# Kernel tuning notes

Hardware: AMD Instinct MI355X
Metric: run time of the kernel (lower is better)

The kernel has to match this reference:

```python
import jax, jax.numpy as jnp
import numpy as np

B, D, K = 32, 64, 26      # batch, n_objects, per-object feature dim
QST = 256                  # question embedding size
G = [512, 512, 512, 512, 512, 512, 28]  # g_layers (last = n_answers)
IN = 2 * K                 # in_size = concat(x_i, x_j)
AGG = 4                    # aggregation + question injection position


def setup_inputs() -> dict:
    key = jax.random.key(0)
    ks = jax.random.split(key, 2 + 2 * len(G))
    inp = {
        "x": jax.random.normal(ks[0], (B, D, K), jnp.float32),
        "qst": jax.random.normal(ks[1], (B, QST), jnp.float32),
    }
    prev = IN
    for i, g in enumerate(G):
        d_in = prev + (QST if i == AGG else 0)
        inp[f"W{i}"] = jax.random.normal(ks[2 + 2 * i], (g, d_in), jnp.float32) * (1.0 / np.sqrt(d_in))
        inp[f"b{i}"] = jnp.zeros((g,), jnp.float32)
        prev = g
    return inp


def reference(x, qst, W0, b0, W1, b1, W2, b2, W3, b3, W4, b4, W5, b5, W6, b6):
    b, d, k = x.shape
    # all ordered pairs: x_full[b, p, q] = [x[b, q], x[b, p]]  (matches torch repeat/cat order)
    xi = jnp.broadcast_to(x[:, None, :, :], (b, d, d, k))
    xj = jnp.broadcast_to(x[:, :, None, :], (b, d, d, k))
    h = jnp.concatenate([xi, xj], axis=-1).reshape(b * d * d, 2 * k)
    Ws = [W0, W1, W2, W3, W4, W5, W6]
    bs = [b0, b1, b2, b3, b4, b5, b6]
    n = len(Ws)
    for i in range(n):
        if i == AGG:
            # sum-aggregation over all d^2 pairs, then question injection
            h = h.reshape(b, d * d, h.shape[-1]).sum(axis=1)  # [b, g]
            h = jnp.concatenate([h, qst], axis=1)             # [b, g+qst]
        h = h @ Ws[i].T + bs[i]
        if i != n - 1:
            h = jax.nn.relu(h)
    return jax.nn.log_softmax(h, axis=1)
```

## Files before the change

### kernel.cpp

```cpp
#include <hip/hip_runtime.h>
#include <math.h>


typedef __attribute__((ext_vector_type(8))) short bf16x8;
typedef __attribute__((ext_vector_type(4))) float f32x4;
typedef __attribute__((ext_vector_type(4))) unsigned int u32x4;

__device__ __forceinline__ unsigned short f2bf(float f) {
    union { float f; unsigned u; } x; x.f = f;
    unsigned r = x.u + 0x7fffu + ((x.u >> 16) & 1u);
    return (unsigned short)(r >> 16);
}

#define NP_WP   786432
#define NP_W0P  32768
#define NP_W4T  393216
#define NP_W5T  262144
#define NP_TOTAL (NP_WP + NP_W0P + NP_W4T + NP_W5T)
__global__ void k_prep(const float* __restrict__ W1, const float* __restrict__ W2,
                       const float* __restrict__ W3, const float* __restrict__ W0,
                       const float* __restrict__ W4, const float* __restrict__ W5,
                       unsigned short* __restrict__ Wp,
                       unsigned short* __restrict__ W0p,
                       float* __restrict__ W4v,
                       float* __restrict__ W5v)
{
    int f = blockIdx.x * 256 + threadIdx.x;
    if (f < NP_WP) {
        int l = f >> 18, r = f & 262143;
        int n = r >> 9, k = r & 511;
        const float* W = (l == 0) ? W1 : (l == 1) ? W2 : W3;
        float v = W[r];
        int wv = n >> 6, jj = (n >> 4) & 3, i16 = n & 15;
        int s = k >> 5, q4 = (k >> 3) & 3, j = k & 7;
        int lane = q4 * 16 + i16;
        Wp[(size_t)l * 262144 + ((((wv * 16 + s) * 4 + jj) * 64 + lane) << 3) + j] = f2bf(v);
    } else if (f < NP_WP + NP_W0P) {
        int g = f - NP_WP;
        int n = g >> 6, k = g & 63;
        float v = (k < 52) ? W0[n * 52 + k] : 0.f;
        int wv = n >> 6, jj = (n >> 4) & 3, i16 = n & 15;
        int s = k >> 5, q4 = (k >> 3) & 3, j = k & 7;
        int lane = q4 * 16 + i16;
        W0p[((((wv * 2 + s) * 4 + jj) * 64 + lane) << 3) + j] = f2bf(v);
    } else if (f < NP_WP + NP_W0P + NP_W4T) {
        int g = f - (NP_WP + NP_W0P);
        int o = g / 768, k = g % 768;
        W4v[(size_t)((k >> 2) * 512 + o) * 4 + (k & 3)] = W4[g];
    } else {
        int g = f - (NP_WP + NP_W0P + NP_W4T);
        int o = g >> 9, k = g & 511;
        W5v[(size_t)((k >> 2) * 512 + o) * 4 + (k & 3)] = W5[g];
    }
}

__device__ __forceinline__ void store_h(const f32x4 (&acc)[4][4], const float* __restrict__ bl,
                                        unsigned short* hsm, int wave, int i16, int q4, int lane)
{
    char* base = (char*)hsm;
    #pragma unroll
    for (int j = 0; j < 4; ++j) {
        int col = (wave * 4 + j) * 16 + i16;
        int g = col >> 3;
        int e = g & 7;
        float bb = bl[col];
        #pragma unroll
        for (int mt = 0; mt < 4; ++mt) {
            #pragma unroll
            for (int r = 0; r < 4; ++r) {
                int row = mt * 16 + q4 * 4 + r;
                float v = fmaxf(acc[mt][j][r] + bb, 0.f);
                unsigned hv = f2bf(v);
                unsigned sw = (unsigned)__builtin_amdgcn_update_dpp(0, (int)hv, 0xB1, 0xF, 0xF, true);
                if ((lane & 1) == 0) {
                    int slot = row ^ e;
                    *(unsigned*)(base + g * 1024 + slot * 16 + ((col & 7) << 1)) = hv | (sw << 16);
                }
            }
        }
    }
}

#define CLUSTER(AV0, AV1, AV2, AV3, BV, JJ)                                              \
    __builtin_amdgcn_s_setprio(1);                                                      \
    acc[0][JJ] = __builtin_amdgcn_mfma_f32_16x16x32_bf16(AV0, BV, acc[0][JJ], 0, 0, 0); \
    acc[1][JJ] = __builtin_amdgcn_mfma_f32_16x16x32_bf16(AV1, BV, acc[1][JJ], 0, 0, 0); \
    acc[2][JJ] = __builtin_amdgcn_mfma_f32_16x16x32_bf16(AV2, BV, acc[2][JJ], 0, 0, 0); \
    acc[3][JJ] = __builtin_amdgcn_mfma_f32_16x16x32_bf16(AV3, BV, acc[3][JJ], 0, 0, 0); \
    __builtin_amdgcn_s_setprio(0);                                                      \
    __builtin_amdgcn_sched_barrier(0);

__global__ __launch_bounds__(512, 2) void k_fused(
    const float* __restrict__ x,
    const unsigned short* __restrict__ Wp,
    const unsigned short* __restrict__ W0p,
    const float* __restrict__ b0, const float* __restrict__ b1,
    const float* __restrict__ b2, const float* __restrict__ b3,
    float* __restrict__ P)
{
    __shared__ __align__(16) unsigned short hsm[64 * 512];
    __shared__ __align__(16) unsigned short xs[8 * 64 * 8];
    int t = threadIdx.x;
    int blk = blockIdx.x;
    int b = blk >> 6, p = blk & 63;

    {
        int row = t >> 3, gr = t & 7;
        const float* xq = x + (size_t)(b * 64 + row) * 26;
        const float* xp = x + (size_t)(b * 64 + p) * 26;
        unsigned w[4];
        #pragma unroll
        for (int h = 0; h < 4; ++h) {
            int k0 = gr * 8 + h * 2;
            int k1 = k0 + 1;
            float f0 = (k0 < 26) ? xq[k0] : (k0 < 52 ? xp[k0 - 26] : 0.f);
            float f1 = (k1 < 26) ? xq[k1] : (k1 < 52 ? xp[k1 - 26] : 0.f);
            w[h] = (unsigned)f2bf(f0) | ((unsigned)f2bf(f1) << 16);
        }
        *(u32x4*)((char*)xs + gr * 1024 + ((row ^ gr) << 4)) = (u32x4){w[0], w[1], w[2], w[3]};
    }

    int wave = t >> 6, lane = t & 63;
    int i16 = lane & 15, q4 = lane >> 4;

    f32x4 acc[4][4];

    __syncthreads();

    {
        #pragma unroll
        for (int mt = 0; mt < 4; ++mt)
            #pragma unroll
            for (int j = 0; j < 4; ++j)
                acc[mt][j] = (f32x4){0.f, 0.f, 0.f, 0.f};
        const unsigned short* Bb0 = W0p + wave * 4096 + lane * 8;
        const char* xb = (const char*)xs;
        #pragma unroll
        for (int s = 0; s < 2; ++s) {
            bf16x8 bfr[4];
            #pragma unroll
            for (int j = 0; j < 4; ++j)
                bfr[j] = *(const bf16x8*)(Bb0 + s * 2048 + j * 512);
            int g = s * 4 + q4;
            const char* A0 = xb + g * 1024 + ((i16 ^ g) << 4);
            #pragma unroll
            for (int mt = 0; mt < 4; ++mt) {
                bf16x8 a = *(const bf16x8*)(A0 + mt * 256);
                #pragma unroll
                for (int j = 0; j < 4; ++j)
                    acc[mt][j] = __builtin_amdgcn_mfma_f32_16x16x32_bf16(a, bfr[j], acc[mt][j], 0, 0, 0);
            }
        }
        store_h(acc, b0, hsm, wave, i16, q4, lane);
    }

    int A_even = (q4 << 10) + ((i16 ^ q4) << 4);
    const char* hbe = (const char*)hsm + A_even;
    const char* hbo = (const char*)hsm + 4096 + (A_even ^ 64);

    #pragma unroll 1
    for (int l = 0; l < 3; ++l) {
        const float* bl = (l == 0) ? b1 : (l == 1) ? b2 : b3;
        const unsigned short* Bb = Wp + (size_t)l * 262144 + wave * 32768 + lane * 8;

        bf16x8 X0 = *(const bf16x8*)(Bb);
        bf16x8 X1 = *(const bf16x8*)(Bb + 512);
        bf16x8 X2 = *(const bf16x8*)(Bb + 1024);
        bf16x8 X3 = *(const bf16x8*)(Bb + 1536);
        bf16x8 Y0 = *(const bf16x8*)(Bb + 2048);
        bf16x8 Y1 = *(const bf16x8*)(Bb + 2560);
        bf16x8 Y2 = *(const bf16x8*)(Bb + 3072);
        bf16x8 Y3 = *(const bf16x8*)(Bb + 3584);

        __syncthreads();

        #pragma unroll
        for (int mt = 0; mt < 4; ++mt)
            #pragma unroll
            for (int j = 0; j < 4; ++j)
                acc[mt][j] = (f32x4){0.f, 0.f, 0.f, 0.f};

        bf16x8 aE0 = *(const bf16x8*)(hbe);
        bf16x8 aE1 = *(const bf16x8*)(hbe + 256);
        bf16x8 aE2 = *(const bf16x8*)(hbe + 512);
        bf16x8 aE3 = *(const bf16x8*)(hbe + 768);
        bf16x8 aO0, aO1, aO2, aO3;

        #pragma unroll 1
        for (int s = 0; s < 16; s += 2) {
            {
                const unsigned short* BX = Bb + ((s + 2 < 16) ? (s + 2) : 14) * 2048;
                const char* po = hbo + (s << 12);
                CLUSTER(aE0, aE1, aE2, aE3, X0, 0)
                X0 = *(const bf16x8*)(BX);
                aO0 = *(const bf16x8*)(po);
                aO1 = *(const bf16x8*)(po + 256);
                CLUSTER(aE0, aE1, aE2, aE3, X1, 1)
                X1 = *(const bf16x8*)(BX + 512);
                aO2 = *(const bf16x8*)(po + 512);
                aO3 = *(const bf16x8*)(po + 768);
                CLUSTER(aE0, aE1, aE2, aE3, X2, 2)
                X2 = *(const bf16x8*)(BX + 1024);
                CLUSTER(aE0, aE1, aE2, aE3, X3, 3)
                X3 = *(const bf16x8*)(BX + 1536);
            }
            {
                const unsigned short* BY = Bb + ((s + 3 < 16) ? (s + 3) : 15) * 2048;
                const char* pe = hbe + ((s + 2 < 16 ? s + 2 : 14) << 12);
                CLUSTER(aO0, aO1, aO2, aO3, Y0, 0)
                Y0 = *(const bf16x8*)(BY);
                aE0 = *(const bf16x8*)(pe);
                aE1 = *(const bf16x8*)(pe + 256);
                CLUSTER(aO0, aO1, aO2, aO3, Y1, 1)
                Y1 = *(const bf16x8*)(BY + 512);
                aE2 = *(const bf16x8*)(pe + 512);
                aE3 = *(const bf16x8*)(pe + 768);
                CLUSTER(aO0, aO1, aO2, aO3, Y2, 2)
                Y2 = *(const bf16x8*)(BY + 1024);
                CLUSTER(aO0, aO1, aO2, aO3, Y3, 3)
                Y3 = *(const bf16x8*)(BY + 1536);
            }
        }
        __syncthreads();

        if (l < 2) {
            store_h(acc, bl, hsm, wave, i16, q4, lane);
        } else {
            #pragma unroll
            for (int j = 0; j < 4; ++j) {
                int col = (wave * 4 + j) * 16 + i16;
                float bb = bl[col];
                float sum = 0.f;
                #pragma unroll
                for (int mt = 0; mt < 4; ++mt)
                    #pragma unroll
                    for (int r = 0; r < 4; ++r)
                        sum += fmaxf(acc[mt][j][r] + bb, 0.f);
                sum += __shfl_xor(sum, 16);
                sum += __shfl_xor(sum, 32);
                if (q4 == 0) P[(size_t)blk * 512 + col] = sum;
            }
        }
    }
}

__global__ __launch_bounds__(1024) void k_tail(
    const float* __restrict__ P, const float* __restrict__ qst,
    const float* __restrict__ W4v, const float* __restrict__ b4,
    const float* __restrict__ W5v, const float* __restrict__ b5,
    const float* __restrict__ W6, const float* __restrict__ b6,
    float* __restrict__ out)
{
    int b = blockIdx.x, t = threadIdx.x;
    __shared__ __align__(16) float z[768];
    __shared__ __align__(16) float ps[1024];
    __shared__ __align__(16) float h4[512];
    __shared__ float h5[512];
    __shared__ float logits[28];
    __shared__ float red[2];

    if (t < 512) {
        float s = 0.f;
        const float* Pb = P + (size_t)b * 64 * 512 + t;
        #pragma unroll 8
        for (int c = 0; c < 64; ++c) s += Pb[c * 512];
        z[t] = s;
    } else if (t < 768) {
        z[t] = qst[b * 256 + (t - 512)];
    }
    __syncthreads();
    {
        int o = t & 511, hf = t >> 9;
        float acc = 0.f;
        const float4* Wv = (const float4*)W4v;
        const float4* z4 = (const float4*)z;
        #pragma unroll 4
        for (int kb = hf * 96; kb < hf * 96 + 96; ++kb) {
            float4 w = Wv[kb * 512 + o];
            float4 zz = z4[kb];
            acc = fmaf(w.x, zz.x, acc);
            acc = fmaf(w.y, zz.y, acc);
            acc = fmaf(w.z, zz.z, acc);
            acc = fmaf(w.w, zz.w, acc);
        }
        ps[t] = acc;
    }
    __syncthreads();
    if (t < 512) h4[t] = fmaxf(ps[t] + ps[t + 512] + b4[t], 0.f);
    __syncthreads();
    {
        int o = t & 511, hf = t >> 9;
        float acc = 0.f;
        const float4* Wv = (const float4*)W5v;
        const float4* h44 = (const float4*)h4;
        #pragma unroll 4
        for (int kb = hf * 64; kb < hf * 64 + 64; ++kb) {
            float4 w = Wv[kb * 512 + o];
            float4 hh = h44[kb];
            acc = fmaf(w.x, hh.x, acc);
            acc = fmaf(w.y, hh.y, acc);
            acc = fmaf(w.z, hh.z, acc);
            acc = fmaf(w.w, hh.w, acc);
        }
        ps[t] = acc;
    }
    __syncthreads();
    if (t < 512) h5[t] = fmaxf(ps[t] + ps[t + 512] + b5[t], 0.f);
    __syncthreads();
    {
        int o = t >> 5, c = t & 31;
        if (o < 28) {
            float acc = 0.f;
            for (int k = c; k < 512; k += 32) acc = fmaf(W6[o * 512 + k], h5[k], acc);
            acc += __shfl_xor(acc, 1);
            acc += __shfl_xor(acc, 2);
            acc += __shfl_xor(acc, 4);
            acc += __shfl_xor(acc, 8);
            acc += __shfl_xor(acc, 16);
            if (c == 0) logits[o] = acc + b6[o];
        }
    }
    __syncthreads();
    if (t == 0) {
        float mx = -1e30f;
        for (int cc = 0; cc < 28; ++cc) mx = fmaxf(mx, logits[cc]);
        float se = 0.f;
        for (int cc = 0; cc < 28; ++cc) se += expf(logits[cc] - mx);
        red[0] = mx; red[1] = logf(se);
    }
    __syncthreads();
    if (t < 28) out[b * 28 + t] = logits[t] - red[0] - red[1];
}

extern "C" void kernel_launch(void* const* d_in, const int* in_sizes, int n_in,
                              void* d_out, int out_size, void* d_ws, size_t ws_size,
                              hipStream_t stream)
{
    const float* x   = (const float*)d_in[0];
    const float* qst = (const float*)d_in[1];
    const float* W0  = (const float*)d_in[2];
    const float* b0  = (const float*)d_in[3];
    const float* W1  = (const float*)d_in[4];
    const float* b1  = (const float*)d_in[5];
    const float* W2  = (const float*)d_in[6];
    const float* b2  = (const float*)d_in[7];
    const float* W3  = (const float*)d_in[8];
    const float* b3  = (const float*)d_in[9];
    const float* W4  = (const float*)d_in[10];
    const float* b4  = (const float*)d_in[11];
    const float* W5  = (const float*)d_in[12];
    const float* b5  = (const float*)d_in[13];
    const float* W6  = (const float*)d_in[14];
    const float* b6  = (const float*)d_in[15];
    float* out = (float*)d_out;

    char* ws = (char*)d_ws;
    unsigned short* Wp  = (unsigned short*)(ws);
    unsigned short* W0p = (unsigned short*)(ws + 1572864);
    float*          W4v = (float*)(ws + 1638400);
    float*          W5v = (float*)(ws + 3211264);
    float*          P   = (float*)(ws + 4259840);

    k_prep <<<NP_TOTAL / 256, 256, 0, stream>>>(W1, W2, W3, W0, W4, W5,
                                                Wp, W0p, W4v, W5v);
    k_fused<<<2048, 512, 0, stream>>>(x, Wp, W0p, b0, b1, b2, b3, P);
    k_tail <<<32, 1024, 0, stream>>>(P, qst, W4v, b4, W5v, b5, W6, b6, out);
}
```

Measured before the change: 324.9 us.

## Deepen register prefetch pipeline to four stages and use packed bf16 convert

The inner GEMM loop for layers 1-3 now keeps four sets of weight and activation register fragments in flight instead of two. It prefetches weights four k-steps ahead and activations three steps ahead, so global and LDS load latency is better hidden behind MFMA clusters. store_h now uses the hardware v_cvt_pk_bf16_f32 instruction instead of manual rounding and bit packing. The deeper pipeline roughly doubles the VGPRs held for fragments, which could cause spills or limit occupancy at 2 blocks of 512 threads.

New measurement: 367.5 us. 13.1% more time.

```diff
diff --git a/kernel.cpp b/kernel.cpp
--- a/kernel.cpp
+++ b/kernel.cpp
@@ -64,17 +64,20 @@
         int g = col >> 3;
         int e = g & 7;
         float bb = bl[col];
+        char* colbase = base + g * 1024 + ((col & 7) << 1);
         #pragma unroll
         for (int mt = 0; mt < 4; ++mt) {
             #pragma unroll
             for (int r = 0; r < 4; ++r) {
                 int row = mt * 16 + q4 * 4 + r;
                 float v = fmaxf(acc[mt][j][r] + bb, 0.f);
-                unsigned hv = f2bf(v);
-                unsigned sw = (unsigned)__builtin_amdgcn_update_dpp(0, (int)hv, 0xB1, 0xF, 0xF, true);
+                int vi = __float_as_int(v);
+                int swi = __builtin_amdgcn_update_dpp(0, vi, 0xB1, 0xF, 0xF, true);
                 if ((lane & 1) == 0) {
+                    unsigned pk;
+                    asm("v_cvt_pk_bf16_f32 %0, %1, %2" : "=v"(pk) : "v"(vi), "v"(swi));
                     int slot = row ^ e;
-                    *(unsigned*)(base + g * 1024 + slot * 16 + ((col & 7) << 1)) = hv | (sw << 16);
+                    *(unsigned*)(colbase + slot * 16) = pk;
                 }
             }
         }
@@ -90,6 +93,20 @@
     __builtin_amdgcn_s_setprio(0);                                                      \
     __builtin_amdgcn_sched_barrier(0);
 
+#define BODY(cA0,cA1,cA2,cA3, cB0,cB1,cB2,cB3, nA0,nA1,nA2,nA3, An, Bn)  \
+    CLUSTER(cA0,cA1,cA2,cA3, cB0, 0)                                     \
+    cB0 = *(const bf16x8*)(Bn);                                          \
+    nA0 = *(const bf16x8*)(An);                                          \
+    nA1 = *(const bf16x8*)((An) + 256);                                  \
+    CLUSTER(cA0,cA1,cA2,cA3, cB1, 1)                                     \
+    cB1 = *(const bf16x8*)((Bn) + 512);                                  \
+    nA2 = *(const bf16x8*)((An) + 512);                                  \
+    nA3 = *(const bf16x8*)((An) + 768);                                  \
+    CLUSTER(cA0,cA1,cA2,cA3, cB2, 2)                                     \
+    cB2 = *(const bf16x8*)((Bn) + 1024);                                 \
+    CLUSTER(cA0,cA1,cA2,cA3, cB3, 3)                                     \
+    cB3 = *(const bf16x8*)((Bn) + 1536);
+
 __global__ __launch_bounds__(512, 2) void k_fused(
     const float* __restrict__ x,
     const unsigned short* __restrict__ Wp,
@@ -156,21 +173,29 @@
 
     int A_even = (q4 << 10) + ((i16 ^ q4) << 4);
     const char* hbe = (const char*)hsm + A_even;
-    const char* hbo = (const char*)hsm + 4096 + (A_even ^ 64);
+    const char* hbo = (const char*)hsm + (A_even ^ 64);
 
     #pragma unroll 1
     for (int l = 0; l < 3; ++l) {
         const float* bl = (l == 0) ? b1 : (l == 1) ? b2 : b3;
         const unsigned short* Bb = Wp + (size_t)l * 262144 + wave * 32768 + lane * 8;
 
-        bf16x8 X0 = *(const bf16x8*)(Bb);
-        bf16x8 X1 = *(const bf16x8*)(Bb + 512);
-        bf16x8 X2 = *(const bf16x8*)(Bb + 1024);
-        bf16x8 X3 = *(const bf16x8*)(Bb + 1536);
-        bf16x8 Y0 = *(const bf16x8*)(Bb + 2048);
-        bf16x8 Y1 = *(const bf16x8*)(Bb + 2560);
-        bf16x8 Y2 = *(const bf16x8*)(Bb + 3072);
-        bf16x8 Y3 = *(const bf16x8*)(Bb + 3584);
+        bf16x8 bX0 = *(const bf16x8*)(Bb);
+        bf16x8 bX1 = *(const bf16x8*)(Bb + 512);
+        bf16x8 bX2 = *(const bf16x8*)(Bb + 1024);
+        bf16x8 bX3 = *(const bf16x8*)(Bb + 1536);
+        bf16x8 bY0 = *(const bf16x8*)(Bb + 2048);
+        bf16x8 bY1 = *(const bf16x8*)(Bb + 2560);
+        bf16x8 bY2 = *(const bf16x8*)(Bb + 3072);
+        bf16x8 bY3 = *(const bf16x8*)(Bb + 3584);
+        bf16x8 bZ0 = *(const bf16x8*)(Bb + 4096);
+        bf16x8 bZ1 = *(const bf16x8*)(Bb + 4608);
+        bf16x8 bZ2 = *(const bf16x8*)(Bb + 5120);
+        bf16x8 bZ3 = *(const bf16x8*)(Bb + 5632);
+        bf16x8 bW0 = *(const bf16x8*)(Bb + 6144);
+        bf16x8 bW1 = *(const bf16x8*)(Bb + 6656);
+        bf16x8 bW2 = *(const bf16x8*)(Bb + 7168);
+        bf16x8 bW3 = *(const bf16x8*)(Bb + 7680);
 
         __syncthreads();
 
@@ -180,46 +205,42 @@
             for (int j = 0; j < 4; ++j)
                 acc[mt][j] = (f32x4){0.f, 0.f, 0.f, 0.f};
 
-        bf16x8 aE0 = *(const bf16x8*)(hbe);
-        bf16x8 aE1 = *(const bf16x8*)(hbe + 256);
-        bf16x8 aE2 = *(const bf16x8*)(hbe + 512);
-        bf16x8 aE3 = *(const bf16x8*)(hbe + 768);
-        bf16x8 aO0, aO1, aO2, aO3;
+        bf16x8 aA0 = *(const bf16x8*)(hbe);
+        bf16x8 aA1 = *(const bf16x8*)(hbe + 256);
+        bf16x8 aA2 = *(const bf16x8*)(hbe + 512);
+        bf16x8 aA3 = *(const bf16x8*)(hbe + 768);
+        const char* a1p = hbo + 4096;
+        bf16x8 aB0 = *(const bf16x8*)(a1p);
+        bf16x8 aB1 = *(const bf16x8*)(a1p + 256);
+        bf16x8 aB2 = *(const bf16x8*)(a1p + 512);
+        bf16x8 aB3 = *(const bf16x8*)(a1p + 768);
+        const char* a2p = hbe + 8192;
+        bf16x8 aC0 = *(const bf16x8*)(a2p);
+        bf16x8 aC1 = *(const bf16x8*)(a2p + 256);
+        bf16x8 aC2 = *(const bf16x8*)(a2p + 512);
+        bf16x8 aC3 = *(const bf16x8*)(a2p + 768);
+        bf16x8 aD0, aD1, aD2, aD3;
 
         #pragma unroll 1
-        for (int s = 0; s < 16; s += 2) {
-            {
-                const unsigned short* BX = Bb + ((s + 2 < 16) ? (s + 2) : 14) * 2048;
-                const char* po = hbo + (s << 12);
-                CLUSTER(aE0, aE1, aE2, aE3, X0, 0)
-                X0 = *(const bf16x8*)(BX);
-                aO0 = *(const bf16x8*)(po);
-                aO1 = *(const bf16x8*)(po + 256);
-                CLUSTER(aE0, aE1, aE2, aE3, X1, 1)
-                X1 = *(const bf16x8*)(BX + 512);
-                aO2 = *(const bf16x8*)(po + 512);
-                aO3 = *(const bf16x8*)(po + 768);
-                CLUSTER(aE0, aE1, aE2, aE3, X2, 2)
-                X2 = *(const bf16x8*)(BX + 1024);
-                CLUSTER(aE0, aE1, aE2, aE3, X3, 3)
-                X3 = *(const bf16x8*)(BX + 1536);
-            }
-            {
-                const unsigned short* BY = Bb + ((s + 3 < 16) ? (s + 3) : 15) * 2048;
-                const char* pe = hbe + ((s + 2 < 16 ? s + 2 : 14) << 12);
-                CLUSTER(aO0, aO1, aO2, aO3, Y0, 0)
-                Y0 = *(const bf16x8*)(BY);
-                aE0 = *(const bf16x8*)(pe);
-                aE1 = *(const bf16x8*)(pe + 256);
-                CLUSTER(aO0, aO1, aO2, aO3, Y1, 1)
-                Y1 = *(const bf16x8*)(BY + 512);
-                aE2 = *(const bf16x8*)(pe + 512);
-                aE3 = *(const bf16x8*)(pe + 768);
-                CLUSTER(aO0, aO1, aO2, aO3, Y2, 2)
-                Y2 = *(const bf16x8*)(BY + 1024);
-                CLUSTER(aO0, aO1, aO2, aO3, Y3, 3)
-                Y3 = *(const bf16x8*)(BY + 1536);
-            }
+        for (int s = 0; s < 16; s += 4) {
+            int sA1 = (s + 4 < 16) ? s + 4 : 12;
+            int sA2 = (s + 5 < 16) ? s + 5 : 13;
+            int sA3 = (s + 6 < 16) ? s + 6 : 14;
+            int sB0 = sA1, sB1 = sA2, sB2 = sA3;
+            int sB3 = (s + 7 < 16) ? s + 7 : 15;
+            const char* An0 = hbo + ((s + 3) << 12);
+            const char* An1 = hbe + (sA1 << 12);
+            const char* An2 = hbo + (sA2 << 12);
+            const char* An3 = hbe + (sA3 << 12);
+            const unsigned short* Bn0 = Bb + sB0 * 2048;
+            const unsigned short* Bn1 = Bb + sB1 * 2048;
+            const unsigned short* Bn2 = Bb + sB2 * 2048;
+            const unsigned short* Bn3 = Bb + sB3 * 2048;
+
+            BODY(aA0,aA1,aA2,aA3, bX0,bX1,bX2,bX3, aD0,aD1,aD2,aD3, An0, Bn0)
+            BODY(aB0,aB1,aB2,aB3, bY0,bY1,bY2,bY3, aA0,aA1,aA2,aA3, An1, Bn1)
+            BODY(aC0,aC1,aC2,aC3, bZ0,bZ1,bZ2,bZ3, aB0,aB1,aB2,aB3, An2, Bn2)
+            BODY(aD0,aD1,aD2,aD3, bW0,bW1,bW2,bW3, aC0,aC1,aC2,aC3, An3, Bn3)
         }
         __syncthreads();
 
```

## Double per-block row tile to 128 pairs to halve weight traffic per MFMA

Applied to the files above, without the earlier changes.

Each block now handles two p values (128 rows) instead of one, doubling the accumulator tile to 8x4 MFMA tiles per wave so every loaded weight fragment feeds twice as many MFMAs. The LDS activation buffer doubles to 128 KB, the inner loop is rescheduled to stream A fragments per row tile, and the grid is halved to 1024 blocks. The bf16 packing in store_h now uses a single v_cvt_pk_bf16_f32 instruction. This raises register and LDS pressure, which may cut occupancy below two blocks per CU.

After: 497.4 us. 1.53x slower.

```diff
diff --git a/kernel.cpp b/kernel.cpp
--- a/kernel.cpp
+++ b/kernel.cpp
@@ -54,7 +54,7 @@
     }
 }
 
-__device__ __forceinline__ void store_h(const f32x4 (&acc)[4][4], const float* __restrict__ bl,
+__device__ __forceinline__ void store_h(const f32x4 (&acc)[8][4], const float* __restrict__ bl,
                                         unsigned short* hsm, int wave, int i16, int q4, int lane)
 {
     char* base = (char*)hsm;
@@ -64,30 +64,33 @@
         int g = col >> 3;
         int e = g & 7;
         float bb = bl[col];
-        #pragma unroll
-        for (int mt = 0; mt < 4; ++mt) {
+        char* colbase = base + g * 2048 + ((col & 7) << 1);
+        #pragma unroll
+        for (int mt = 0; mt < 8; ++mt) {
             #pragma unroll
             for (int r = 0; r < 4; ++r) {
                 int row = mt * 16 + q4 * 4 + r;
                 float v = fmaxf(acc[mt][j][r] + bb, 0.f);
-                unsigned hv = f2bf(v);
-                unsigned sw = (unsigned)__builtin_amdgcn_update_dpp(0, (int)hv, 0xB1, 0xF, 0xF, true);
+                int vi = __float_as_int(v);
+                int swi = __builtin_amdgcn_update_dpp(0, vi, 0xB1, 0xF, 0xF, true);
                 if ((lane & 1) == 0) {
+                    unsigned pk;
+                    asm("v_cvt_pk_bf16_f32 %0, %1, %2" : "=v"(pk) : "v"(vi), "v"(swi));
                     int slot = row ^ e;
-                    *(unsigned*)(base + g * 1024 + slot * 16 + ((col & 7) << 1)) = hv | (sw << 16);
+                    *(unsigned*)(colbase + slot * 16) = pk;
                 }
             }
         }
     }
 }
 
-#define CLUSTER(AV0, AV1, AV2, AV3, BV, JJ)                                              \
-    __builtin_amdgcn_s_setprio(1);                                                      \
-    acc[0][JJ] = __builtin_amdgcn_mfma_f32_16x16x32_bf16(AV0, BV, acc[0][JJ], 0, 0, 0); \
-    acc[1][JJ] = __builtin_amdgcn_mfma_f32_16x16x32_bf16(AV1, BV, acc[1][JJ], 0, 0, 0); \
-    acc[2][JJ] = __builtin_amdgcn_mfma_f32_16x16x32_bf16(AV2, BV, acc[2][JJ], 0, 0, 0); \
-    acc[3][JJ] = __builtin_amdgcn_mfma_f32_16x16x32_bf16(AV3, BV, acc[3][JJ], 0, 0, 0); \
-    __builtin_amdgcn_s_setprio(0);                                                      \
+#define CLUSTER(AV, B0v, B1v, B2v, B3v, MT)                                               \
+    __builtin_amdgcn_s_setprio(1);                                                       \
+    acc[MT][0] = __builtin_amdgcn_mfma_f32_16x16x32_bf16(AV, B0v, acc[MT][0], 0, 0, 0);  \
+    acc[MT][1] = __builtin_amdgcn_mfma_f32_16x16x32_bf16(AV, B1v, acc[MT][1], 0, 0, 0);  \
+    acc[MT][2] = __builtin_amdgcn_mfma_f32_16x16x32_bf16(AV, B2v, acc[MT][2], 0, 0, 0);  \
+    acc[MT][3] = __builtin_amdgcn_mfma_f32_16x16x32_bf16(AV, B3v, acc[MT][3], 0, 0, 0);  \
+    __builtin_amdgcn_s_setprio(0);                                                       \
     __builtin_amdgcn_sched_barrier(0);
 
 __global__ __launch_bounds__(512, 2) void k_fused(
@@ -98,38 +101,44 @@
     const float* __restrict__ b2, const float* __restrict__ b3,
     float* __restrict__ P)
 {
-    __shared__ __align__(16) unsigned short hsm[64 * 512];
-    __shared__ __align__(16) unsigned short xs[8 * 64 * 8];
+    __shared__ __align__(16) unsigned short hsm[128 * 512];
+    __shared__ __align__(16) unsigned short xs[8 * 128 * 8];
     int t = threadIdx.x;
     int blk = blockIdx.x;
-    int b = blk >> 6, p = blk & 63;
-
-    {
-        int row = t >> 3, gr = t & 7;
-        const float* xq = x + (size_t)(b * 64 + row) * 26;
-        const float* xp = x + (size_t)(b * 64 + p) * 26;
-        unsigned w[4];
-        #pragma unroll
-        for (int h = 0; h < 4; ++h) {
-            int k0 = gr * 8 + h * 2;
-            int k1 = k0 + 1;
-            float f0 = (k0 < 26) ? xq[k0] : (k0 < 52 ? xp[k0 - 26] : 0.f);
-            float f1 = (k1 < 26) ? xq[k1] : (k1 < 52 ? xp[k1 - 26] : 0.f);
-            w[h] = (unsigned)f2bf(f0) | ((unsigned)f2bf(f1) << 16);
-        }
-        *(u32x4*)((char*)xs + gr * 1024 + ((row ^ gr) << 4)) = (u32x4){w[0], w[1], w[2], w[3]};
+    int b = blk >> 5, pw = blk & 31;
+
+    {
+        int row = t >> 2, sub = t & 3;
+        int q = row & 63;
+        int pp = (pw << 1) + (row >> 6);
+        const float* xq = x + (size_t)(b * 64 + q) * 26;
+        const float* xp = x + (size_t)(b * 64 + pp) * 26;
+        #pragma unroll
+        for (int gi = 0; gi < 2; ++gi) {
+            int g = sub * 2 + gi;
+            unsigned w[4];
+            #pragma unroll
+            for (int h = 0; h < 4; ++h) {
+                int k0 = g * 8 + h * 2;
+                int k1 = k0 + 1;
+                float f0 = (k0 < 26) ? xq[k0] : (k0 < 52 ? xp[k0 - 26] : 0.f);
+                float f1 = (k1 < 26) ? xq[k1] : (k1 < 52 ? xp[k1 - 26] : 0.f);
+                w[h] = (unsigned)f2bf(f0) | ((unsigned)f2bf(f1) << 16);
+            }
+            *(u32x4*)((char*)xs + g * 2048 + ((row ^ g) << 4)) = (u32x4){w[0], w[1], w[2], w[3]};
+        }
     }
 
     int wave = t >> 6, lane = t & 63;
     int i16 = lane & 15, q4 = lane >> 4;
 
-    f32x4 acc[4][4];
-
-    __syncthreads();
-
-    {
-        #pragma unroll
-        for (int mt = 0; mt < 4; ++mt)
+    f32x4 acc[8][4];
+
+    __syncthreads();
+
+    {
+        #pragma unroll
+        for (int mt = 0; mt < 8; ++mt)
             #pragma unroll
             for (int j = 0; j < 4; ++j)
                 acc[mt][j] = (f32x4){0.f, 0.f, 0.f, 0.f};
@@ -142,9 +151,9 @@
             for (int j = 0; j < 4; ++j)
                 bfr[j] = *(const bf16x8*)(Bb0 + s * 2048 + j * 512);
             int g = s * 4 + q4;
-            const char* A0 = xb + g * 1024 + ((i16 ^ g) << 4);
-            #pragma unroll
-            for (int mt = 0; mt < 4; ++mt) {
+            const char* A0 = xb + g * 2048 + ((i16 ^ (g & 7)) << 4);
+            #pragma unroll
+            for (int mt = 0; mt < 8; ++mt) {
                 bf16x8 a = *(const bf16x8*)(A0 + mt * 256);
                 #pragma unroll
                 for (int j = 0; j < 4; ++j)
@@ -154,9 +163,9 @@
         store_h(acc, b0, hsm, wave, i16, q4, lane);
     }
 
-    int A_even = (q4 << 10) + ((i16 ^ q4) << 4);
-    const char* hbe = (const char*)hsm + A_even;
-    const char* hbo = (const char*)hsm + 4096 + (A_even ^ 64);
+    int A_evenoff = (q4 << 11) + ((i16 ^ q4) << 4);
+    const char* hbe = (const char*)hsm + A_evenoff;
+    const char* hbo = (const char*)hsm + (A_evenoff ^ 64);
 
     #pragma unroll 1
     for (int l = 0; l < 3; ++l) {
@@ -175,51 +184,54 @@
         __syncthreads();
 
         #pragma unroll
-        for (int mt = 0; mt < 4; ++mt)
+        for (int mt = 0; mt < 8; ++mt)
             #pragma unroll
             for (int j = 0; j < 4; ++j)
                 acc[mt][j] = (f32x4){0.f, 0.f, 0.f, 0.f};
 
-        bf16x8 aE0 = *(const bf16x8*)(hbe);
-        bf16x8 aE1 = *(const bf16x8*)(hbe + 256);
-        bf16x8 aE2 = *(const bf16x8*)(hbe + 512);
-        bf16x8 aE3 = *(const bf16x8*)(hbe + 768);
-        bf16x8 aO0, aO1, aO2, aO3;
+        bf16x8 A0 = *(const bf16x8*)(hbe);
+        bf16x8 A1 = *(const bf16x8*)(hbe + 256);
+        bf16x8 A2 = *(const bf16x8*)(hbe + 512);
+        bf16x8 A3 = *(const bf16x8*)(hbe + 768);
+        bf16x8 A4 = *(const bf16x8*)(hbe + 1024);
+        bf16x8 A5 = *(const bf16x8*)(hbe + 1280);
+        bf16x8 A6 = *(const bf16x8*)(hbe + 1536);
+        bf16x8 A7 = *(const bf16x8*)(hbe + 1792);
 
         #pragma unroll 1
         for (int s = 0; s < 16; s += 2) {
-            {
-                const unsigned short* BX = Bb + ((s + 2 < 16) ? (s + 2) : 14) * 2048;
-                const char* po = hbo + (s << 12);
-                CLUSTER(aE0, aE1, aE2, aE3, X0, 0)
-                X0 = *(const bf16x8*)(BX);
-                aO0 = *(const bf16x8*)(po);
-                aO1 = *(const bf16x8*)(po + 256);
-                CLUSTER(aE0, aE1, aE2, aE3, X1, 1)
-                X1 = *(const bf16x8*)(BX + 512);
-                aO2 = *(const bf16x8*)(po + 512);
-                aO3 = *(const bf16x8*)(po + 768);
-                CLUSTER(aE0, aE1, aE2, aE3, X2, 2)
-                X2 = *(const bf16x8*)(BX + 1024);
-                CLUSTER(aE0, aE1, aE2, aE3, X3, 3)
-                X3 = *(const bf16x8*)(BX + 1536);
-            }
-            {
-                const unsigned short* BY = Bb + ((s + 3 < 16) ? (s + 3) : 15) * 2048;
-                const char* pe = hbe + ((s + 2 < 16 ? s + 2 : 14) << 12);
-                CLUSTER(aO0, aO1, aO2, aO3, Y0, 0)
-                Y0 = *(const bf16x8*)(BY);
-                aE0 = *(const bf16x8*)(pe);
-                aE1 = *(const bf16x8*)(pe + 256);
-                CLUSTER(aO0, aO1, aO2, aO3, Y1, 1)
-                Y1 = *(const bf16x8*)(BY + 512);
-                aE2 = *(const bf16x8*)(pe + 512);
-                aE3 = *(const bf16x8*)(pe + 768);
-                CLUSTER(aO0, aO1, aO2, aO3, Y2, 2)
-                Y2 = *(const bf16x8*)(BY + 1024);
-                CLUSTER(aO0, aO1, aO2, aO3, Y3, 3)
-                Y3 = *(const bf16x8*)(BY + 1536);
-            }
+            int s2 = (s + 2 < 16) ? s + 2 : 14;
+            int s3 = (s + 3 < 16) ? s + 3 : 15;
+            const char* pnO = hbo + ((s + 1) << 13);
+            const char* pnE = hbe + (s2 << 13);
+            const unsigned short* BX = Bb + s2 * 2048;
+            const unsigned short* BY = Bb + s3 * 2048;
+
+            CLUSTER(A0, X0, X1, X2, X3, 0)  A0 = *(const bf16x8*)(pnO);
+            CLUSTER(A1, X0, X1, X2, X3, 1)  A1 = *(const bf16x8*)(pnO + 256);
+            CLUSTER(A2, X0, X1, X2, X3, 2)  A2 = *(const bf16x8*)(pnO + 512);
+            CLUSTER(A3, X0, X1, X2, X3, 3)  A3 = *(const bf16x8*)(pnO + 768);
+            CLUSTER(A4, X0, X1, X2, X3, 4)  A4 = *(const bf16x8*)(pnO + 1024);
+            CLUSTER(A5, X0, X1, X2, X3, 5)  A5 = *(const bf16x8*)(pnO + 1280);
+            CLUSTER(A6, X0, X1, X2, X3, 6)  A6 = *(const bf16x8*)(pnO + 1536);
+            CLUSTER(A7, X0, X1, X2, X3, 7)  A7 = *(const bf16x8*)(pnO + 1792);
+
+            X0 = *(const bf16x8*)(BX);
+            X1 = *(const bf16x8*)(BX + 512);
+            X2 = *(const bf16x8*)(BX + 1024);
+            X3 = *(const bf16x8*)(BX + 1536);
+            CLUSTER(A0, Y0, Y1, Y2, Y3, 0)  A0 = *(const bf16x8*)(pnE);
+            CLUSTER(A1, Y0, Y1, Y2, Y3, 1)  A1 = *(const bf16x8*)(pnE + 256);
+            CLUSTER(A2, Y0, Y1, Y2, Y3, 2)  A2 = *(const bf16x8*)(pnE + 512);
+            CLUSTER(A3, Y0, Y1, Y2, Y3, 3)  A3 = *(const bf16x8*)(pnE + 768);
+            CLUSTER(A4, Y0, Y1, Y2, Y3, 4)  A4 = *(const bf16x8*)(pnE + 1024);
+            CLUSTER(A5, Y0, Y1, Y2, Y3, 5)  A5 = *(const bf16x8*)(pnE + 1280);
+            CLUSTER(A6, Y0, Y1, Y2, Y3, 6)  A6 = *(const bf16x8*)(pnE + 1536);
+            CLUSTER(A7, Y0, Y1, Y2, Y3, 7)  A7 = *(const bf16x8*)(pnE + 1792);
+            Y0 = *(const bf16x8*)(BY);
+            Y1 = *(const bf16x8*)(BY + 512);
+            Y2 = *(const bf16x8*)(BY + 1024);
+            Y3 = *(const bf16x8*)(BY + 1536);
         }
         __syncthreads();
 
@@ -232,7 +244,7 @@
                 float bb = bl[col];
                 float sum = 0.f;
                 #pragma unroll
-                for (int mt = 0; mt < 4; ++mt)
+                for (int mt = 0; mt < 8; ++mt)
                     #pragma unroll
                     for (int r = 0; r < 4; ++r)
                         sum += fmaxf(acc[mt][j][r] + bb, 0.f);
@@ -261,9 +273,9 @@
 
     if (t < 512) {
         float s = 0.f;
-        const float* Pb = P + (size_t)b * 64 * 512 + t;
+        const float* Pb = P + (size_t)b * 32 * 512 + t;
         #pragma unroll 8
-        for (int c = 0; c < 64; ++c) s += Pb[c * 512];
+        for (int c = 0; c < 32; ++c) s += Pb[c * 512];
         z[t] = s;
     } else if (t < 768) {
         z[t] = qst[b * 256 + (t - 512)];
@@ -363,6 +375,6 @@
 
     k_prep <<<NP_TOTAL / 256, 256, 0, stream>>>(W1, W2, W3, W0, W4, W5,
                                                 Wp, W0p, W4v, W5v);
-    k_fused<<<2048, 512, 0, stream>>>(x, Wp, W0p, b0, b1, b2, b3, P);
+    k_fused<<<1024, 512, 0, stream>>>(x, Wp, W0p, b0, b1, b2, b3, P);
     k_tail <<<32, 1024, 0, stream>>>(P, qst, W4v, b4, W5v, b5, W6, b6, out);
 }
```
